# Optimization experiments

Measured on AMD Instinct MI355X. Metric: run time of the kernel, lower is better.

## Reference

```python
import jax, jax.numpy as jnp
import numpy as np

B, S, D = 4, 2048, 512
H, HD, RL = 8, 64, 64   # nheads, head_dim = D//H, rl_dim
TEMPER = 1.0
BETA = 1.0
SLOPE = 0.01  # LeakyReLU negative slope
LN_EPS = 1e-5


def setup_inputs() -> dict:
    key = jax.random.key(0)
    ks = jax.random.split(key, 12)
    scale = 0.02
    return {
        "h":   jax.random.normal(ks[0], (B, S, D), dtype=jnp.float32),
        "rh":  jax.random.normal(ks[1], (B, S, RL), dtype=jnp.float32),
        "Wl":  jax.random.normal(ks[2], (D, D), dtype=jnp.float32) * scale,   # linear_l (in,out)
        "Wr":  jax.random.normal(ks[3], (D, D), dtype=jnp.float32) * scale,   # linear_r
        "al":  jax.random.normal(ks[4], (HD,), dtype=jnp.float32) * scale,    # att_l: Linear(head_dim,1)
        "ar":  jax.random.normal(ks[5], (HD,), dtype=jnp.float32) * scale,    # att_r
        "Wrs": jax.random.normal(ks[6], (RL, RL * H), dtype=jnp.float32) * scale,  # r_source
        "Wrt": jax.random.normal(ks[7], (RL, RL * H), dtype=jnp.float32) * scale,  # r_target
        "Wf":  jax.random.normal(ks[8], (D, D), dtype=jnp.float32) * scale,   # linear_final
        "ln_g": jnp.ones((D,), dtype=jnp.float32),
        "ln_b": jnp.zeros((D,), dtype=jnp.float32),
    }


def _layer_norm(x, g, b):
    mu = jnp.mean(x, axis=-1, keepdims=True)
    var = jnp.mean(jnp.square(x - mu), axis=-1, keepdims=True)
    return (x - mu) * jax.lax.rsqrt(var + LN_EPS) * g + b


def reference(h, rh, Wl, Wr, al, ar, Wrs, Wrt, Wf, ln_g, ln_b):
    leaky = lambda x: jnp.where(x >= 0, x, SLOPE * x)
    # projections -> [B, H, S, HD]
    fl = (h @ Wl).reshape(B, S, H, HD).transpose(0, 2, 1, 3)
    fr = (h @ Wr).reshape(B, S, H, HD).transpose(0, 2, 1, 3)
    # additive attention logits: [B,H,S,1] + [B,H,1,S]
    sl = jnp.einsum('bhsd,d->bhs', leaky(fl), al)
    sr = jnp.einsum('bhsd,d->bhs', leaky(fr), ar)
    score = sl[:, :, :, None] + sr[:, :, None, :]
    # relation-embedding bilinear bias: r_k @ r_q -> [B,H,S,S]
    r_k = (rh @ Wrs).reshape(B, S, H, RL).transpose(0, 2, 1, 3)   # [B,H,S,RL]
    r_q = (rh @ Wrt).reshape(B, S, H, RL).transpose(0, 2, 3, 1)   # [B,H,RL,S]
    score = score + BETA * jnp.einsum('bhsr,bhrt->bhst', r_k, r_q)
    score = jax.nn.softmax(score / TEMPER, axis=-1)
    # context and output projection (dropout = 0 -> identity)
    context = jnp.einsum('bhst,bhtd->bhsd', score, fr)
    h_sa = context.transpose(0, 2, 1, 3).reshape(B, S, H * HD)
    fh = h_sa @ Wf
    return _layer_norm(h + fh, ln_g, ln_b)
```

## Files before the change

### kernel.cpp

```cpp
#include <hip/hip_runtime.h>
#include <math.h>

#define B_ 4
#define S_ 2048
#define D_ 512
#define H_ 8
#define HD_ 64
#define RL_ 64
#define LN_EPS 1e-5f
#define SLOPE 0.01f
#define LOG2E 1.4426950408889634f

typedef __attribute__((ext_vector_type(8))) __bf16 bf16x8;
typedef __attribute__((ext_vector_type(4))) float f32x4;
typedef __attribute__((ext_vector_type(16))) float f32x16;

__device__ __forceinline__ float leaky(float x) { return x >= 0.f ? x : SLOPE * x; }

__device__ __forceinline__ ushort f2bf(float f) {
    union { float f; unsigned u; } v; v.f = f;
    unsigned r = v.u + 0x7fffu + ((v.u >> 16) & 1u);
    return (ushort)(r >> 16);
}
__device__ __forceinline__ unsigned pk2bf(float a, float b) {
    return (unsigned)f2bf(a) | ((unsigned)f2bf(b) << 16);
}

__device__ __forceinline__ void g2lds16(const void* g, void* l) {
    __builtin_amdgcn_global_load_lds(
        (const __attribute__((address_space(1))) void*)(uintptr_t)g,
        (__attribute__((address_space(3))) void*)(uintptr_t)l, 16, 0, 0);
}

__device__ __forceinline__ void plane32swap(unsigned &x, unsigned &y) {
    asm volatile("v_permlane32_swap_b32 %0, %1" : "+v"(x), "+v"(y));
}

__global__ __launch_bounds__(256) void prep(
    const float* __restrict__ h, const float* __restrict__ rh,
    const float* __restrict__ Wr, const float* __restrict__ Wf,
    const float* __restrict__ Wrs, const float* __restrict__ Wrt,
    ushort* __restrict__ hb, ushort* __restrict__ rhb,
    ushort* __restrict__ WrT, ushort* __restrict__ WfT,
    ushort* __restrict__ WrsT, ushort* __restrict__ WrtT)
{
    const int bx = blockIdx.x, tid = threadIdx.x;
    if (bx < 4608) {
        const float* in = (bx < 4096) ? h : rh;
        ushort* o = (bx < 4096) ? hb : rhb;
        const int i = (bx < 4096 ? bx : bx - 4096) * 256 + tid;
        const float4 v = ((const float4*)in)[i];
        ushort4 u; u.x = f2bf(v.x); u.y = f2bf(v.y); u.z = f2bf(v.z); u.w = f2bf(v.w);
        ((ushort4*)o)[i] = u;
        return;
    }
    __shared__ float TS[64][65];
    int t = bx - 4608;
    const float* in; ushort* out; int K, tk, tn;
    if (t < 64)       { in = Wr;  out = WrT;  K = 512; tk = t & 7; tn = t >> 3; }
    else if (t < 128) { in = Wf;  out = WfT;  K = 512; t -= 64; tk = t & 7; tn = t >> 3; }
    else if (t < 136) { in = Wrs; out = WrsT; K = 64;  tk = 0; tn = t - 128; }
    else              { in = Wrt; out = WrtT; K = 64;  tk = 0; tn = t - 136; }
    const int k0 = tk * 64, n0 = tn * 64;
    const int r = tid >> 4, c4 = (tid & 15) * 4;
    #pragma unroll
    for (int p = 0; p < 4; ++p) {
        const int row = r + 16 * p;
        const float4 v = *(const float4*)(in + (size_t)(k0 + row) * 512 + n0 + c4);
        TS[row][c4] = v.x; TS[row][c4 + 1] = v.y;
        TS[row][c4 + 2] = v.z; TS[row][c4 + 3] = v.w;
    }
    __syncthreads();
    #pragma unroll
    for (int p = 0; p < 4; ++p) {
        const int nn = r + 16 * p;
        ushort4 o;
        o.x = f2bf(TS[c4 + 0][nn]); o.y = f2bf(TS[c4 + 1][nn]);
        o.z = f2bf(TS[c4 + 2][nn]); o.w = f2bf(TS[c4 + 3][nn]);
        *(ushort4*)(out + (size_t)(n0 + nn) * K + k0 + c4) = o;
    }
}

__global__ __launch_bounds__(256) void proj(
    const ushort* __restrict__ hb, const ushort* __restrict__ rhb,
    const ushort* __restrict__ WrT, const ushort* __restrict__ WrsT,
    const ushort* __restrict__ WrtT,
    ushort* __restrict__ frT, ushort* __restrict__ rkw, ushort* __restrict__ rqw,
    float* __restrict__ sred, const float* __restrict__ ar)
{
    __shared__ ushort As[2][64 * 32];
    __shared__ ushort Bs[2][128 * 32];

    const int tid = threadIdx.x;
    const int lane = tid & 63, w = tid >> 6;
    const int ln = lane & 15, quad = lane >> 4;
    const int wm = w >> 1, wn = w & 1;
    const int m0 = blockIdx.x * 64, n0 = blockIdx.y * 128;
    const int z = blockIdx.z;

    const ushort* A; const ushort* wt; ushort* co; float scl; int K;
    if (z == 0)      { A = hb;  wt = WrT;  co = frT; scl = LOG2E; K = 512; }
    else if (z == 1) { A = rhb; wt = WrsT; co = rkw; scl = LOG2E; K = 64; }
    else             { A = rhb; wt = WrtT; co = rqw; scl = 1.0f;  K = 64; }

    const int srA = tid >> 2;
    const int lchA = ((lane & 3) - (srA >> 1)) & 3;
    const ushort* AgB = A + (size_t)(m0 + srA) * K + lchA * 8;
    const int srB = w * 32 + (lane >> 2);
    const int lchB = ((lane & 3) - (srB >> 1)) & 3;
    const ushort* BgB0 = wt + (size_t)(n0 + srB) * K + lchB * 8;
    const ushort* BgB1 = BgB0 + (size_t)16 * K;
    const int aoff = tid * 8;
    const int boff = srB * 32 + (lane & 3) * 8;
    const int pc = (quad + (ln >> 1)) & 3;

    g2lds16(AgB, &As[0][aoff]);
    g2lds16(BgB0, &Bs[0][boff]);
    g2lds16(BgB1, &Bs[0][boff + 512]);

    f32x4 acc[2][4] = {};
    int buf = 0;
    for (int k0 = 0; k0 < K; k0 += 32) {
        __syncthreads();
        if (k0 + 32 < K) {
            g2lds16(AgB + k0 + 32, &As[buf ^ 1][aoff]);
            g2lds16(BgB0 + k0 + 32, &Bs[buf ^ 1][boff]);
            g2lds16(BgB1 + k0 + 32, &Bs[buf ^ 1][boff + 512]);
        }
        bf16x8 af[2], bfr[4];
        #pragma unroll
        for (int mi = 0; mi < 2; ++mi)
            af[mi] = *(const bf16x8*)&As[buf][(wm * 32 + mi * 16 + ln) * 32 + pc * 8];
        #pragma unroll
        for (int ni = 0; ni < 4; ++ni)
            bfr[ni] = *(const bf16x8*)&Bs[buf][(wn * 64 + ni * 16 + ln) * 32 + pc * 8];
        #pragma unroll
        for (int mi = 0; mi < 2; ++mi)
            #pragma unroll
            for (int ni = 0; ni < 4; ++ni)
                acc[mi][ni] = __builtin_amdgcn_mfma_f32_16x16x32_bf16(
                    af[mi], bfr[ni], acc[mi][ni], 0, 0, 0);
        buf ^= 1;
    }

    const int head = blockIdx.y * 2 + wn;
    const int b = m0 >> 11;
    const size_t bh = (size_t)b * H_ + head;
    if (z == 0) {
        #pragma unroll
        for (int mi = 0; mi < 2; ++mi) {
            const int s = (m0 & (S_ - 1)) + wm * 32 + mi * 16 + quad * 4;
            const int sp = (s & ~15) | ((((0x1320u >> (quad * 4)) & 0xFu)) << 2);
            #pragma unroll
            for (int ni = 0; ni < 4; ++ni) {
                const int d = ni * 16 + ln;
                ushort4 o;
                o.x = f2bf(acc[mi][ni][0]); o.y = f2bf(acc[mi][ni][1]);
                o.z = f2bf(acc[mi][ni][2]); o.w = f2bf(acc[mi][ni][3]);
                *(ushort4*)(co + (bh * 64 + d) * S_ + sp) = o;
            }
        }
        float a4[4];
        #pragma unroll
        for (int ni = 0; ni < 4; ++ni) a4[ni] = ar[ni * 16 + ln];
        #pragma unroll
        for (int mi = 0; mi < 2; ++mi) {
            const int s = (m0 & (S_ - 1)) + wm * 32 + mi * 16 + quad * 4;
            #pragma unroll
            for (int r = 0; r < 4; ++r) {
                float v = 0.f;
                #pragma unroll
                for (int ni = 0; ni < 4; ++ni)
                    v += leaky(acc[mi][ni][r]) * a4[ni];
                #pragma unroll
                for (int off = 8; off; off >>= 1) v += __shfl_xor(v, off, 16);
                if (ln == 0) sred[bh * S_ + s + r] = v * scl;
            }
        }
    } else {
        #pragma unroll
        for (int mi = 0; mi < 2; ++mi) {
            const int s = (m0 & (S_ - 1)) + wm * 32 + mi * 16 + quad * 4;
            #pragma unroll
            for (int ni = 0; ni < 4; ++ni) {
                const int d = ni * 16 + ln;
                #pragma unroll
                for (int r = 0; r < 4; ++r)
                    co[(bh * S_ + s + r) * 64 + d] = f2bf(acc[mi][ni][r] * scl);
            }
        }
    }
}

#define WAITV(N) asm volatile("s_waitcnt vmcnt(" #N ")" ::: "memory")
#define BARR()   __builtin_amdgcn_s_barrier()

__global__ __launch_bounds__(128, 1) void attn_mfma(
    const ushort* __restrict__ frT, const ushort* __restrict__ rk,
    const ushort* __restrict__ rq, const float* __restrict__ sr,
    ushort* __restrict__ hsa)
{
    __shared__ ushort RQ[2][64][64];
    __shared__ ushort FT[2][64][64];

    const int tid = threadIdx.x;
    const int w = tid >> 6;
    const int lane = tid & 63;
    const int lq = lane & 31;
    const int hi = lane >> 5;

    const int flat = blockIdx.x + 16 * (blockIdx.y + 8 * blockIdx.z);
    const int wid = (flat & 7) * 64 + (flat >> 3);
    const int q0 = (wid & 15) * 128;
    const int h = (wid >> 4) & 7;
    const int b = wid >> 7;
    const size_t bh = (size_t)b * H_ + h;
    const int qb = q0 + 64 * w;

    bf16x8 bq[2][4];
    #pragma unroll
    for (int qt = 0; qt < 2; ++qt) {
        const ushort* p = rk + ((bh * S_ + qb + 32 * qt + lq) << 6) + hi * 8;
        #pragma unroll
        for (int ks = 0; ks < 4; ++ks)
            bq[qt][ks] = *(const bf16x8*)(p + ks * 16);
    }

    const ushort* rq_g = rq + (bh * S_ << 6);
    const ushort* ft_g = frT + (size_t)bh * 64 * S_;
    const float* srp = sr + bh * S_;

    const int srow = tid >> 3;
    const int pg = tid & 7;
    const int oS = (pg - (srow & 7)) & 7;

    #define STAGE(BUF, t0)                                                    \
        { _Pragma("unroll")                                                   \
          for (int j = 0; j < 4; ++j) {                                       \
            const int rr = 16 * j + srow;                                     \
            g2lds16(rq_g + ((size_t)((t0) + rr) << 6) + oS * 8,               \
                    &RQ[BUF][rr][pg * 8]);                                    \
            g2lds16(ft_g + (size_t)rr * S_ + (t0) + oS * 8,                   \
                    &FT[BUF][rr][pg * 8]);                                    \
          } }

    f32x16 ctx[2][2] = {};
    float lsum[2] = {0.f, 0.f};

    #define COMPUTE(BI, TC)                                                    \
    {                                                                          \
        uint4 paw[2][4];                                                       \
        _Pragma("unroll")                                                      \
        for (int tt = 0; tt < 2; ++tt) {                                       \
            bf16x8 af[4];                                                      \
            _Pragma("unroll")                                                  \
            for (int ks = 0; ks < 4; ++ks)                                     \
                af[ks] = *(const bf16x8*)(&RQ[BI][0][0] + (tt * 32 + lq) * 64  \
                           + ((2 * ks + hi + (lq & 7)) & 7) * 8);              \
            f32x16 s0 = {}; f32x16 s1 = {};                                    \
            _Pragma("unroll")                                                  \
            for (int ks = 0; ks < 4; ++ks) {                                   \
                s0 = __builtin_amdgcn_mfma_f32_32x32x16_bf16(af[ks], bq[0][ks], s0, 0, 0, 0); \
                s1 = __builtin_amdgcn_mfma_f32_32x32x16_bf16(af[ks], bq[1][ks], s1, 0, 0, 0); \
            }                                                                  \
            float sva[16];                                                     \
            _Pragma("unroll")                                                  \
            for (int jj = 0; jj < 4; ++jj) {                                   \
                const float4 v = *(const float4*)(srp + (TC) + tt * 32 + jj * 8 + hi * 4); \
                sva[jj * 4 + 0] = v.x; sva[jj * 4 + 1] = v.y;                  \
                sva[jj * 4 + 2] = v.z; sva[jj * 4 + 3] = v.w;                  \
            }                                                                  \
            _Pragma("unroll")                                                  \
            for (int qt = 0; qt < 2; ++qt) {                                   \
                float p[16];                                                   \
                _Pragma("unroll")                                              \
                for (int r = 0; r < 16; ++r)                                   \
                    p[r] = __builtin_amdgcn_exp2f((qt ? s1[r] : s0[r]) + sva[r]); \
                float ls = 0.f;                                                \
                _Pragma("unroll")                                              \
                for (int r = 0; r < 16; ++r) ls += p[r];                       \
                lsum[qt] += ls;                                                \
                _Pragma("unroll")                                              \
                for (int c = 0; c < 2; ++c) {                                  \
                    const int e = 8 * c;                                       \
                    unsigned c01 = pk2bf(p[e + 0], p[e + 1]);                  \
                    unsigned c23 = pk2bf(p[e + 2], p[e + 3]);                  \
                    unsigned c45 = pk2bf(p[e + 4], p[e + 5]);                  \
                    unsigned c67 = pk2bf(p[e + 6], p[e + 7]);                  \
                    plane32swap(c45, c67);   \
                    paw[qt][tt * 2 + c] = make_uint4(c01, c23, c67, c45);      \
                }                                                              \
            }                                                                  \
        }                                                                      \
        _Pragma("unroll")                                                      \
        for (int ts = 0; ts < 4; ++ts) {                                       \
            _Pragma("unroll")                                                  \
            for (int dt = 0; dt < 2; ++dt) {                                   \
                const bf16x8 fv = *(const bf16x8*)(&FT[BI][0][0]               \
                    + (dt * 32 + lq) * 64 + ((2 * ts + hi + (lq & 7)) & 7) * 8); \
                ctx[0][dt] = __builtin_amdgcn_mfma_f32_32x32x16_bf16(          \
                    __builtin_bit_cast(bf16x8, paw[0][ts]), fv, ctx[0][dt], 0, 0, 0); \
                ctx[1][dt] = __builtin_amdgcn_mfma_f32_32x32x16_bf16(          \
                    __builtin_bit_cast(bf16x8, paw[1][ts]), fv, ctx[1][dt], 0, 0, 0); \
            }                                                                  \
        }                                                                      \
    }

    STAGE(0, 0)
    for (int it = 0; it < 15; ++it) {
        const int t0 = it * 128;
        WAITV(0); BARR();
        STAGE(1, t0 + 64)
        COMPUTE(0, t0)
        WAITV(0); BARR();
        STAGE(0, t0 + 128)
        COMPUTE(1, t0 + 64)
    }
    WAITV(0); BARR();
    STAGE(1, 1984)
    COMPUTE(0, 1920)
    WAITV(0); BARR();
    COMPUTE(1, 1984)

    #pragma unroll
    for (int qt = 0; qt < 2; ++qt) {
        const float l = lsum[qt] + __shfl_xor(lsum[qt], 32, 64);
        const float inv = 1.f / l;
        #pragma unroll
        for (int r = 0; r < 16; ++r) {
            const int rho = (r & 3) + 8 * (r >> 2) + 4 * hi;
            const float fi = __shfl(inv, rho, 64);
            const int q = qb + 32 * qt + rho;
            ushort* orow = hsa + (size_t)(b * S_ + q) * D_ + h * 64 + lq;
            orow[0]  = f2bf(ctx[qt][0][r] * fi);
            orow[32] = f2bf(ctx[qt][1][r] * fi);
        }
    }
}

__global__ __launch_bounds__(256) void gemm_out(
    const ushort* __restrict__ A, const ushort* __restrict__ WT,
    float* __restrict__ C)
{
    __shared__ ushort As[2][64 * 32];
    __shared__ ushort Bs[2][128 * 32];

    const int tid = threadIdx.x;
    const int lane = tid & 63, w = tid >> 6;
    const int ln = lane & 15, quad = lane >> 4;
    const int wm = w >> 1, wn = w & 1;
    const int m0 = blockIdx.x * 64, n0 = blockIdx.y * 128;
    const int K = 512;

    const int srA = tid >> 2;
    const int lchA = ((lane & 3) - (srA >> 1)) & 3;
    const ushort* AgB = A + (size_t)(m0 + srA) * K + lchA * 8;
    const int srB = w * 32 + (lane >> 2);
    const int lchB = ((lane & 3) - (srB >> 1)) & 3;
    const ushort* BgB0 = WT + (size_t)(n0 + srB) * K + lchB * 8;
    const ushort* BgB1 = BgB0 + (size_t)16 * K;
    const int aoff = tid * 8;
    const int boff = srB * 32 + (lane & 3) * 8;
    const int pc = (quad + (ln >> 1)) & 3;

    g2lds16(AgB, &As[0][aoff]);
    g2lds16(BgB0, &Bs[0][boff]);
    g2lds16(BgB1, &Bs[0][boff + 512]);

    f32x4 acc[2][4] = {};
    int buf = 0;
    for (int k0 = 0; k0 < K; k0 += 32) {
        __syncthreads();
        if (k0 + 32 < K) {
            g2lds16(AgB + k0 + 32, &As[buf ^ 1][aoff]);
            g2lds16(BgB0 + k0 + 32, &Bs[buf ^ 1][boff]);
            g2lds16(BgB1 + k0 + 32, &Bs[buf ^ 1][boff + 512]);
        }
        bf16x8 af[2], bfr[4];
        #pragma unroll
        for (int mi = 0; mi < 2; ++mi)
            af[mi] = *(const bf16x8*)&As[buf][(wm * 32 + mi * 16 + ln) * 32 + pc * 8];
        #pragma unroll
        for (int ni = 0; ni < 4; ++ni)
            bfr[ni] = *(const bf16x8*)&Bs[buf][(wn * 64 + ni * 16 + ln) * 32 + pc * 8];
        #pragma unroll
        for (int mi = 0; mi < 2; ++mi)
            #pragma unroll
            for (int ni = 0; ni < 4; ++ni)
                acc[mi][ni] = __builtin_amdgcn_mfma_f32_16x16x32_bf16(
                    af[mi], bfr[ni], acc[mi][ni], 0, 0, 0);
        buf ^= 1;
    }

    #pragma unroll
    for (int mi = 0; mi < 2; ++mi) {
        const int row = m0 + wm * 32 + mi * 16 + quad * 4;
        #pragma unroll
        for (int ni = 0; ni < 4; ++ni) {
            const int col = n0 + wn * 64 + ni * 16 + ln;
            #pragma unroll
            for (int r = 0; r < 4; ++r)
                C[(size_t)(row + r) * 512 + col] = acc[mi][ni][r];
        }
    }
}

__global__ __launch_bounds__(256) void ln_kernel(
    const float* __restrict__ h, const float* __restrict__ fh,
    const float* __restrict__ g, const float* __restrict__ bb,
    float* __restrict__ out)
{
    const int row = blockIdx.x, tid = threadIdx.x;
    const float* hp = h + (size_t)row * 512;
    const float* fp = fh + (size_t)row * 512;
    const float x0 = hp[tid] + fp[tid];
    const float x1 = hp[tid + 256] + fp[tid + 256];
    __shared__ float red[4];

    float s = x0 + x1;
    #pragma unroll
    for (int off = 32; off; off >>= 1) s += __shfl_xor(s, off, 64);
    if ((tid & 63) == 0) red[tid >> 6] = s;
    __syncthreads();
    const float mu = (red[0] + red[1] + red[2] + red[3]) * (1.f / 512.f);

    const float d0 = x0 - mu, d1 = x1 - mu;
    float v = d0 * d0 + d1 * d1;
    #pragma unroll
    for (int off = 32; off; off >>= 1) v += __shfl_xor(v, off, 64);
    __syncthreads();
    if ((tid & 63) == 0) red[tid >> 6] = v;
    __syncthreads();
    const float var = (red[0] + red[1] + red[2] + red[3]) * (1.f / 512.f);
    const float inv = rsqrtf(var + LN_EPS);

    out[(size_t)row * 512 + tid] = d0 * inv * g[tid] + bb[tid];
    out[(size_t)row * 512 + tid + 256] = d1 * inv * g[tid + 256] + bb[tid + 256];
}

extern "C" void kernel_launch(void* const* d_in, const int* in_sizes, int n_in,
                              void* d_out, int out_size, void* d_ws, size_t ws_size,
                              hipStream_t stream)
{
    const float* h   = (const float*)d_in[0];
    const float* rh  = (const float*)d_in[1];
    const float* Wr  = (const float*)d_in[3];
    const float* ar  = (const float*)d_in[5];
    const float* Wrs = (const float*)d_in[6];
    const float* Wrt = (const float*)d_in[7];
    const float* Wf  = (const float*)d_in[8];
    const float* lng = (const float*)d_in[9];
    const float* lnb = (const float*)d_in[10];
    float* out = (float*)d_out;
    char* wsb  = (char*)d_ws;

    const size_t MB = (size_t)1 << 20;
    ushort* hb   = (ushort*)(wsb);
    ushort* rhb  = (ushort*)(wsb + 8 * MB);
    ushort* WrT  = (ushort*)(wsb + 9 * MB);
    ushort* WfT  = (ushort*)(wsb + 9 * MB + 512 * 1024);
    ushort* WrsT = (ushort*)(wsb + 10 * MB);
    ushort* WrtT = (ushort*)(wsb + 10 * MB + 64 * 1024);
    ushort* frT  = (ushort*)(wsb + 11 * MB);
    ushort* rkw  = (ushort*)(wsb + 19 * MB);
    ushort* rqw  = (ushort*)(wsb + 27 * MB);
    float*  sr   = (float*) (wsb + 35 * MB);
    ushort* hsab = (ushort*)(wsb + 36 * MB);
    float*  fh   = (float*) (wsb + 44 * MB);

    dim3 blk(256);
    prep<<<dim3(4752), blk, 0, stream>>>(h, rh, Wr, Wf, Wrs, Wrt,
                                         hb, rhb, WrT, WfT, WrsT, WrtT);
    proj<<<dim3(128, 4, 3), blk, 0, stream>>>(hb, rhb, WrT, WrsT, WrtT,
                                              frT, rkw, rqw, sr, ar);
    attn_mfma<<<dim3(S_ / 128, H_, B_), dim3(128), 0, stream>>>(frT, rkw, rqw, sr, hsab);
    gemm_out<<<dim3(128, 4), blk, 0, stream>>>(hsab, WfT, fh);
    ln_kernel<<<dim3(B_ * S_), blk, 0, stream>>>(h, fh, lng, lnb, out);
}
```

Before: 197.2 us.

## Split key tiles across two waves per query group and use hardware bf16 pack

The attention kernel now runs 256 threads per block. Each pair of waves shares a 64-query group and splits each 64-key tile in half, so every wave does half the score MFMAs, exps and context MFMAs per tile. The partial context accumulators and row sums are combined through LDS at the end. The software float-to-bf16 rounding in the probability packing is replaced with the v_cvt_pk_bf16_f32 instruction. This doubles the waves available to hide latency, at the cost of an extra LDS reduction and barrier at the epilogue and fewer global loads per thread during staging.

Result: slower. 204.6 us (+3.8%).

```diff
diff --git a/kernel.cpp b/kernel.cpp
--- a/kernel.cpp
+++ b/kernel.cpp
@@ -22,8 +22,10 @@
     unsigned r = v.u + 0x7fffu + ((v.u >> 16) & 1u);
     return (ushort)(r >> 16);
 }
-__device__ __forceinline__ unsigned pk2bf(float a, float b) {
-    return (unsigned)f2bf(a) | ((unsigned)f2bf(b) << 16);
+__device__ __forceinline__ unsigned cvtpk(float a, float b) {
+    unsigned r;
+    asm("v_cvt_pk_bf16_f32 %0, %1, %2" : "=v"(r) : "v"(a), "v"(b));
+    return r;
 }
 
 __device__ __forceinline__ void g2lds16(const void* g, void* l) {
@@ -195,16 +197,20 @@
 #define WAITV(N) asm volatile("s_waitcnt vmcnt(" #N ")" ::: "memory")
 #define BARR()   __builtin_amdgcn_s_barrier()
 
-__global__ __launch_bounds__(128, 1) void attn_mfma(
+__global__ __launch_bounds__(256, 1) void attn_mfma(
     const ushort* __restrict__ frT, const ushort* __restrict__ rk,
     const ushort* __restrict__ rq, const float* __restrict__ sr,
     ushort* __restrict__ hsa)
 {
-    __shared__ ushort RQ[2][64][64];
-    __shared__ ushort FT[2][64][64];
+    __shared__ ushort SMEM[16384];
+    __shared__ float  LS[4][2][64];
+    ushort* RQp = SMEM;
+    ushort* FTp = SMEM + 8192;
 
     const int tid = threadIdx.x;
     const int w = tid >> 6;
+    const int qg = w >> 1;
+    const int th = w & 1;
     const int lane = tid & 63;
     const int lq = lane & 31;
     const int hi = lane >> 5;
@@ -215,7 +221,7 @@
     const int h = (wid >> 4) & 7;
     const int b = wid >> 7;
     const size_t bh = (size_t)b * H_ + h;
-    const int qb = q0 + 64 * w;
+    const int qb = q0 + 64 * qg;
 
     bf16x8 bq[2][4];
     #pragma unroll
@@ -236,12 +242,12 @@
 
     #define STAGE(BUF, t0)                                                    \
         { _Pragma("unroll")                                                   \
-          for (int j = 0; j < 4; ++j) {                                       \
-            const int rr = 16 * j + srow;                                     \
+          for (int j = 0; j < 2; ++j) {                                       \
+            const int rr = 32 * j + srow;                                     \
             g2lds16(rq_g + ((size_t)((t0) + rr) << 6) + oS * 8,               \
-                    &RQ[BUF][rr][pg * 8]);                                    \
+                    RQp + (BUF) * 4096 + rr * 64 + pg * 8);                   \
             g2lds16(ft_g + (size_t)rr * S_ + (t0) + oS * 8,                   \
-                    &FT[BUF][rr][pg * 8]);                                    \
+                    FTp + (BUF) * 4096 + rr * 64 + pg * 8);                   \
           } }
 
     f32x16 ctx[2][2] = {};
@@ -249,59 +255,57 @@
 
     #define COMPUTE(BI, TC)                                                    \
     {                                                                          \
-        uint4 paw[2][4];                                                       \
+        bf16x8 af[4];                                                          \
         _Pragma("unroll")                                                      \
-        for (int tt = 0; tt < 2; ++tt) {                                       \
-            bf16x8 af[4];                                                      \
+        for (int ks = 0; ks < 4; ++ks)                                         \
+            af[ks] = *(const bf16x8*)(RQp + (BI) * 4096 + (th * 32 + lq) * 64  \
+                       + ((2 * ks + hi + (lq & 7)) & 7) * 8);                  \
+        f32x16 s0 = {}; f32x16 s1 = {};                                        \
+        _Pragma("unroll")                                                      \
+        for (int ks = 0; ks < 4; ++ks) {                                       \
+            s0 = __builtin_amdgcn_mfma_f32_32x32x16_bf16(af[ks], bq[0][ks], s0, 0, 0, 0); \
+            s1 = __builtin_amdgcn_mfma_f32_32x32x16_bf16(af[ks], bq[1][ks], s1, 0, 0, 0); \
+        }                                                                      \
+        float sva[16];                                                         \
+        _Pragma("unroll")                                                      \
+        for (int jj = 0; jj < 4; ++jj) {                                       \
+            const float4 v = *(const float4*)(srp + (TC) + th * 32 + jj * 8 + hi * 4); \
+            sva[jj * 4 + 0] = v.x; sva[jj * 4 + 1] = v.y;                      \
+            sva[jj * 4 + 2] = v.z; sva[jj * 4 + 3] = v.w;                      \
+        }                                                                      \
+        uint4 paw[2][2];                                                       \
+        _Pragma("unroll")                                                      \
+        for (int qt = 0; qt < 2; ++qt) {                                       \
+            float p[16];                                                       \
             _Pragma("unroll")                                                  \
-            for (int ks = 0; ks < 4; ++ks)                                     \
-                af[ks] = *(const bf16x8*)(&RQ[BI][0][0] + (tt * 32 + lq) * 64  \
-                           + ((2 * ks + hi + (lq & 7)) & 7) * 8);              \
-            f32x16 s0 = {}; f32x16 s1 = {};                                    \
+            for (int r = 0; r < 16; ++r)                                       \
+                p[r] = __builtin_amdgcn_exp2f((qt ? s1[r] : s0[r]) + sva[r]);  \
+            float ls = 0.f;                                                    \
             _Pragma("unroll")                                                  \
-            for (int ks = 0; ks < 4; ++ks) {                                   \
-                s0 = __builtin_amdgcn_mfma_f32_32x32x16_bf16(af[ks], bq[0][ks], s0, 0, 0, 0); \
-                s1 = __builtin_amdgcn_mfma_f32_32x32x16_bf16(af[ks], bq[1][ks], s1, 0, 0, 0); \
-            }                                                                  \
-            float sva[16];                                                     \
+            for (int r = 0; r < 16; ++r) ls += p[r];                           \
+            lsum[qt] += ls;                                                    \
             _Pragma("unroll")                                                  \
-            for (int jj = 0; jj < 4; ++jj) {                                   \
-                const float4 v = *(const float4*)(srp + (TC) + tt * 32 + jj * 8 + hi * 4); \
-                sva[jj * 4 + 0] = v.x; sva[jj * 4 + 1] = v.y;                  \
-                sva[jj * 4 + 2] = v.z; sva[jj * 4 + 3] = v.w;                  \
-            }                                                                  \
-            _Pragma("unroll")                                                  \
-            for (int qt = 0; qt < 2; ++qt) {                                   \
-                float p[16];                                                   \
-                _Pragma("unroll")                                              \
-                for (int r = 0; r < 16; ++r)                                   \
-                    p[r] = __builtin_amdgcn_exp2f((qt ? s1[r] : s0[r]) + sva[r]); \
-                float ls = 0.f;                                                \
-                _Pragma("unroll")                                              \
-                for (int r = 0; r < 16; ++r) ls += p[r];                       \
-                lsum[qt] += ls;                                                \
-                _Pragma("unroll")                                              \
-                for (int c = 0; c < 2; ++c) {                                  \
-                    const int e = 8 * c;                                       \
-                    unsigned c01 = pk2bf(p[e + 0], p[e + 1]);                  \
-                    unsigned c23 = pk2bf(p[e + 2], p[e + 3]);                  \
-                    unsigned c45 = pk2bf(p[e + 4], p[e + 5]);                  \
-                    unsigned c67 = pk2bf(p[e + 6], p[e + 7]);                  \
-                    plane32swap(c45, c67);   \
-                    paw[qt][tt * 2 + c] = make_uint4(c01, c23, c67, c45);      \
-                }                                                              \
+            for (int c = 0; c < 2; ++c) {                                      \
+                const int e = 8 * c;                                           \
+                unsigned c01 = cvtpk(p[e + 0], p[e + 1]);                      \
+                unsigned c23 = cvtpk(p[e + 2], p[e + 3]);                      \
+                unsigned c45 = cvtpk(p[e + 4], p[e + 5]);                      \
+                unsigned c67 = cvtpk(p[e + 6], p[e + 7]);                      \
+                plane32swap(c45, c67);                                         \
+                paw[qt][c] = make_uint4(c01, c23, c67, c45);                   \
             }                                                                  \
         }                                                                      \
         _Pragma("unroll")                                                      \
-        for (int ts = 0; ts < 4; ++ts) {                                       \
+        for (int c = 0; c < 2; ++c) {                                          \
             _Pragma("unroll")                                                  \
             for (int dt = 0; dt < 2; ++dt) {                                   \
-                const bf16x8 fv = *(const bf16x8*)(&FT[BI][0][0]               \
-                    + (dt * 32 + lq) * 64 + ((2 * ts + hi + (lq & 7)) & 7) * 8); \
+                const bf16x8 fv = *(const bf16x8*)(FTp + (BI) * 4096           \
+                    + (dt * 32 + lq) * 64                                      \
+                    + ((4 * th + 2 * c + hi + (lq & 7)) & 7) * 8);             \
                 ctx[0][dt] = __builtin_amdgcn_mfma_f32_32x32x16_bf16(          \
-                    __builtin_bit_cast(bf16x8, paw[0][ts]), fv, ctx[0][dt], 0, 0, 0); \
+                    __builtin_bit_cast(bf16x8, paw[0][c]), fv, ctx[0][dt], 0, 0, 0); \
                 ctx[1][dt] = __builtin_amdgcn_mfma_f32_32x32x16_bf16(          \
-                    __builtin_bit_cast(bf16x8, paw[1][ts]), fv, ctx[1][dt], 0, 0, 0); \
+                    __builtin_bit_cast(bf16x8, paw[1][c]), fv, ctx[1][dt], 0, 0, 0); \
             }                                                                  \
         }                                                                      \
     }
@@ -322,18 +326,30 @@
     WAITV(0); BARR();
     COMPUTE(1, 1984)
 
+    BARR();
+    float* CX = (float*)SMEM;
+    float* CXw = CX + w * 2048;
+    #pragma unroll
+    for (int qt = 0; qt < 2; ++qt)
+        #pragma unroll
+        for (int r = 0; r < 16; ++r)
+            CXw[(qt * 16 + r) * 64 + lane] = ctx[qt][1 - th][r];
+    LS[w][0][lane] = lsum[0];
+    LS[w][1][lane] = lsum[1];
+    BARR();
+    const float* CXp = CX + (w ^ 1) * 2048;
     #pragma unroll
     for (int qt = 0; qt < 2; ++qt) {
-        const float l = lsum[qt] + __shfl_xor(lsum[qt], 32, 64);
+        float lt = lsum[qt] + LS[w ^ 1][qt][lane];
+        const float l = lt + __shfl_xor(lt, 32, 64);
         const float inv = 1.f / l;
         #pragma unroll
         for (int r = 0; r < 16; ++r) {
+            const float cv = ctx[qt][th][r] + CXp[(qt * 16 + r) * 64 + lane];
             const int rho = (r & 3) + 8 * (r >> 2) + 4 * hi;
             const float fi = __shfl(inv, rho, 64);
             const int q = qb + 32 * qt + rho;
-            ushort* orow = hsa + (size_t)(b * S_ + q) * D_ + h * 64 + lq;
-            orow[0]  = f2bf(ctx[qt][0][r] * fi);
-            orow[32] = f2bf(ctx[qt][1][r] * fi);
+            hsa[(size_t)(b * S_ + q) * D_ + h * 64 + th * 32 + lq] = f2bf(cv * fi);
         }
     }
 }
@@ -473,7 +489,7 @@
                                          hb, rhb, WrT, WfT, WrsT, WrtT);
     proj<<<dim3(128, 4, 3), blk, 0, stream>>>(hb, rhb, WrT, WrsT, WrtT,
                                               frT, rkw, rqw, sr, ar);
-    attn_mfma<<<dim3(S_ / 128, H_, B_), dim3(128), 0, stream>>>(frT, rkw, rqw, sr, hsab);
+    attn_mfma<<<dim3(S_ / 128, H_, B_), blk, 0, stream>>>(frT, rkw, rqw, sr, hsab);
     gemm_out<<<dim3(128, 4), blk, 0, stream>>>(hsab, WfT, fh);
     ln_kernel<<<dim3(B_ * S_), blk, 0, stream>>>(h, fh, lng, lnb, out);
 }
```
